# Kernel tuning notes

Hardware: AMD Instinct MI355X
Metric: run time of the kernel (lower is better)

## Reference

```python
import jax, jax.numpy as jnp
import numpy as np

# config
HIDDEN = 1024
NUM_EXPERTS = 16
TOP_K = 4
MOE_INTER = 512
NUM_SHARED = 2
SHARED_INTER = MOE_INTER * NUM_SHARED  # 1024
NORM_TOPK = True
ROUTED_SCALE = 1.0
NUM_TOKENS = 1024


def setup_inputs() -> dict:
    key = jax.random.key(0)
    ks = jax.random.split(key, 8)
    s = 0.02
    return {
        "hidden_states": jax.random.normal(ks[0], (NUM_TOKENS, HIDDEN), jnp.float32),
        # router (BailingMoEGate): weight [E, H], no bias
        "router_w": jax.random.normal(ks[1], (NUM_EXPERTS, HIDDEN), jnp.float32) * s,
        # routed experts: gate/up proj [E, H, I], down proj [E, I, H]
        "w_gate": jax.random.normal(ks[2], (NUM_EXPERTS, HIDDEN, MOE_INTER), jnp.float32) * s,
        "w_up": jax.random.normal(ks[3], (NUM_EXPERTS, HIDDEN, MOE_INTER), jnp.float32) * s,
        "w_down": jax.random.normal(ks[4], (NUM_EXPERTS, MOE_INTER, HIDDEN), jnp.float32) * s,
        # shared experts (BailingMoEMLP, merged gate_up): [H, 2*Is], [Is, H]
        "ws_gate_up": jax.random.normal(ks[5], (HIDDEN, 2 * SHARED_INTER), jnp.float32) * s,
        "ws_down": jax.random.normal(ks[6], (SHARED_INTER, HIDDEN), jnp.float32) * s,
    }


def _moe_forward(x, router_w, w_gate, w_up, w_down, ws_gate_up, ws_down):
    T = x.shape[0]
    # ---- router: logits -> softmax -> top-k (score_function='softmax', no bias)
    logits = jnp.einsum("th,eh->te", x, router_w)          # [T, E]
    probs = jax.nn.softmax(logits, axis=-1)
    topk_w, topk_idx = jax.lax.top_k(probs, TOP_K)         # [T, K]
    if NORM_TOPK:
        topk_w = topk_w / jnp.sum(topk_w, axis=-1, keepdims=True)
    topk_w = topk_w * ROUTED_SCALE
    # sparse combine weights [T, E] (zeros for non-selected experts)
    combine = jnp.zeros((T, NUM_EXPERTS), x.dtype).at[
        jnp.arange(T)[:, None], topk_idx
    ].set(topk_w.astype(x.dtype))
    # ---- routed experts: SiLU(x W_gate) * (x W_up) then W_down, weighted combine
    g = jnp.einsum("th,ehi->tei", x, w_gate)               # [T, E, I]
    u = jnp.einsum("th,ehi->tei", x, w_up)
    h = jax.nn.silu(g) * u
    routed = jnp.einsum("tei,eih,te->th", h, w_down, combine)
    # ---- shared experts (dense SwiGLU MLP)
    gu = x @ ws_gate_up                                    # [T, 2*Is]
    g_s, u_s = jnp.split(gu, 2, axis=-1)
    shared = (jax.nn.silu(g_s) * u_s) @ ws_down
    return routed + shared


def reference(hidden_states, router_w, w_gate, w_up, w_down, ws_gate_up, ws_down):
    return _moe_forward(hidden_states, router_w, w_gate, w_up, w_down,
                        ws_gate_up, ws_down)
```

## Files before the change

### kernel.cpp

```cpp
#include <hip/hip_runtime.h>
#include <stdint.h>


typedef __attribute__((ext_vector_type(8))) unsigned short ushort8;
typedef __attribute__((ext_vector_type(4))) float f32x4;
typedef __attribute__((ext_vector_type(8))) __bf16 bf16x8;

#define T_TOK 1024
#define HID   1024
#define NEXP  16
#define TOPK  4
#define MINTER 512
#define SINTER 1024

constexpr size_t OFF_COUNTS = 0;
constexpr size_t OFF_LIST   = 1024;
constexpr size_t OFF_WT     = OFF_LIST  + 65536;
constexpr size_t OFF_TIDX   = OFF_WT    + 65536;
constexpr size_t OFF_XB     = OFF_TIDX  + 65536;
constexpr size_t OFF_HS     = OFF_XB    + 2097152;
constexpr size_t OFF_HR     = OFF_HS    + 2097152;
constexpr size_t OFF_WGT    = OFF_HR    + 4194304;
constexpr size_t OFF_WUT    = OFF_WGT   + 16777216;
constexpr size_t OFF_WDT    = OFF_WUT   + 16777216;
constexpr size_t OFF_WSGUT  = OFF_WDT   + 16777216;
constexpr size_t OFF_WSDT   = OFF_WSGUT + 4194304;
constexpr size_t OFF_ROUT   = OFF_WGT;

__device__ __forceinline__ unsigned short f2bf(float f) {
  union { float f; uint32_t u; } v; v.f = f;
  uint32_t r = (v.u + 0x7FFFu + ((v.u >> 16) & 1u)) >> 16;
  return (unsigned short)r;
}
__device__ __forceinline__ bf16x8 as_bf16x8(ushort8 s) {
  union { ushort8 s; bf16x8 b; } u; u.s = s; return u.b;
}
__device__ __forceinline__ float silu(float g) { return g / (1.f + __expf(-g)); }

__device__ __forceinline__ void glds16(const unsigned short* g, unsigned short* l) {
  __builtin_amdgcn_global_load_lds(
      (const __attribute__((address_space(1))) unsigned int*)g,
      (__attribute__((address_space(3))) unsigned int*)l, 16, 0, 0);
}

__global__ void init_kernel(int* counts) {
  if (threadIdx.x < NEXP) counts[threadIdx.x] = 0;
}

__global__ __launch_bounds__(64) void router_kernel(
    const float* __restrict__ x, const float* __restrict__ rw,
    int* counts, int* list, float* wt, int* tIdx) {
  const int t = blockIdx.x, l = threadIdx.x;
  float xv[16];
#pragma unroll
  for (int j = 0; j < 16; j++) xv[j] = x[t * HID + j * 64 + l];
  float p[NEXP];
#pragma unroll
  for (int e = 0; e < NEXP; e++) {
    float s = 0.f;
#pragma unroll
    for (int j = 0; j < 16; j++) s += xv[j] * rw[e * HID + j * 64 + l];
#pragma unroll
    for (int off = 32; off > 0; off >>= 1) s += __shfl_xor(s, off);
    p[e] = s;
  }
  float mx = p[0];
#pragma unroll
  for (int e = 1; e < NEXP; e++) mx = fmaxf(mx, p[e]);
  int idx[TOPK]; float w4[TOPK]; float wsum = 0.f; unsigned used = 0u;
#pragma unroll
  for (int k = 0; k < TOPK; k++) {
    float bv = -1e30f; int bi = 0;
#pragma unroll
    for (int e = 0; e < NEXP; e++)
      if (!((used >> e) & 1u) && p[e] > bv) { bv = p[e]; bi = e; }
    used |= 1u << bi;
    idx[k] = bi;
    w4[k] = __expf(p[bi] - mx);
    wsum += w4[k];
  }
  const float inv = 1.f / wsum;
  if (l < TOPK) {
    const int e = idx[l];
    const int pos = atomicAdd(&counts[e], 1);
    list[e * 1024 + pos] = t;
    wt[e * 1024 + pos]   = w4[l] * inv;
    tIdx[t * TOPK + l]   = (e << 10) | pos;
  }
}

__global__ void convert_bf16_kernel(const float* __restrict__ src,
                                    unsigned short* __restrict__ dst, int n) {
  const int i = (blockIdx.x * blockDim.x + threadIdx.x) * 4;
  if (i + 3 < n) {
    const float4 v = *(const float4*)(src + i);
    dst[i + 0] = f2bf(v.x); dst[i + 1] = f2bf(v.y);
    dst[i + 2] = f2bf(v.z); dst[i + 3] = f2bf(v.w);
  }
}

__global__ __launch_bounds__(256) void transpose64_kernel(
    const float* __restrict__ src, unsigned short* __restrict__ dst,
    int R, int C) {
  __shared__ float tile[64][65];
  const size_t bo = (size_t)blockIdx.z * R * C;
  const int c0 = blockIdx.x * 64, r0 = blockIdx.y * 64, t = threadIdx.x;
  {
    const int r = t >> 4, c4 = (t & 15) * 4;
#pragma unroll
    for (int p = 0; p < 4; p++) {
      const int rr = p * 16 + r;
      const float4 v = *(const float4*)(src + bo + (size_t)(r0 + rr) * C + c0 + c4);
      tile[rr][c4 + 0] = v.x; tile[rr][c4 + 1] = v.y;
      tile[rr][c4 + 2] = v.z; tile[rr][c4 + 3] = v.w;
    }
  }
  __syncthreads();
  {
    const int c = t >> 2, rb = (t & 3) * 16;
#pragma unroll
    for (int s = 0; s < 4; s++) {
      const int rr = rb + 4 * s;
      union { unsigned short u[4]; uint2 v; } pk;
#pragma unroll
      for (int i = 0; i < 4; i++) pk.u[i] = f2bf(tile[rr + i][c]);
      *(uint2*)(dst + bo + (size_t)(c0 + c) * R + r0 + rr) = pk.v;
    }
  }
}

__global__ __launch_bounds__(256, 2) void phase1_kernel(
    const unsigned short* __restrict__ Xb,
    const unsigned short* __restrict__ WgT,
    const unsigned short* __restrict__ WuT,
    const unsigned short* __restrict__ WsguT,
    const int* __restrict__ counts, const int* __restrict__ list,
    const float* __restrict__ wt,
    unsigned short* __restrict__ Hr,
    unsigned short* __restrict__ Hs) {
  const int z = blockIdx.z, x = blockIdx.x, y = blockIdx.y;
  const bool routed = (z < NEXP);
  int cnt = 0, base = 0;
  if (routed) {
    if (x >= 4) return;
    cnt = counts[z];
    if (y * 128 >= cnt) return;
#pragma unroll
    for (int i = 0; i < NEXP; i++) base += (i < z) ? counts[i] : 0;
  }
  __shared__ __align__(16) unsigned short sA[128 * 64];
  __shared__ __align__(16) unsigned short sB[256 * 64];
  const int tid = threadIdx.x, w = tid >> 6, l = tid & 63;
  const int wm = w >> 1, wn = w & 1, m0 = y * 128;

  const int ar = tid >> 1;
  const unsigned short* aRow;
  if (routed) {
    const int pos = min(m0 + ar, cnt - 1);
    aRow = Xb + (size_t)list[z * 1024 + pos] * HID;
  } else {
    aRow = Xb + (size_t)(m0 + ar) * HID;
  }
  const unsigned short* aptr[4];
  int aoff[4];
#pragma unroll
  for (int c = 0; c < 4; c++) {
    const int p = (tid & 1) * 4 + c;
    aptr[c] = aRow + ((p ^ (ar & 7)) * 8);
    aoff[c] = ar * 64 + p * 8;
  }
  const unsigned short* bptr[8];
#pragma unroll
  for (int i = 0; i < 8; i++) {
    const int R = 64 * w + 8 * i + (l >> 3);
    const int g = (l & 7) ^ (R & 7);
    const unsigned short* rowp;
    if (routed) {
      const int col = x * 128 + (R & 127);
      rowp = ((R >> 7) ? WuT : WgT) + (size_t)z * MINTER * HID + (size_t)col * HID;
    } else {
      const int col = x * 128 + (R & 127);
      rowp = WsguT + (size_t)((R >> 7) * SINTER + col) * HID;
    }
    bptr[i] = rowp + g * 8;
  }

  f32x4 accG[4][4], accU[4][4];
#pragma unroll
  for (int i = 0; i < 4; i++)
#pragma unroll
    for (int j = 0; j < 4; j++) {
      accG[i][j] = (f32x4){0.f, 0.f, 0.f, 0.f};
      accU[i][j] = (f32x4){0.f, 0.f, 0.f, 0.f};
    }

  for (int k0 = 0; k0 < HID; k0 += 64) {
    ushort8 av[4];
#pragma unroll
    for (int c = 0; c < 4; c++) av[c] = *(const ushort8*)(aptr[c] + k0);
    __syncthreads();
#pragma unroll
    for (int c = 0; c < 4; c++) *(ushort8*)(sA + aoff[c]) = av[c];
#pragma unroll
    for (int i = 0; i < 8; i++)
      glds16(bptr[i] + k0, sB + (64 * w + 8 * i) * 64);
    __syncthreads();
#pragma unroll
    for (int h = 0; h < 2; h++) {
      const int pc = ((h * 4 + (l >> 4)) ^ (l & 7)) * 8;
      bf16x8 af[4];
#pragma unroll
      for (int i = 0; i < 4; i++)
        af[i] = as_bf16x8(*(const ushort8*)(sA + (wm * 64 + 16 * i + (l & 15)) * 64 + pc));
#pragma unroll
      for (int j = 0; j < 4; j++) {
        const int Rg = wn * 64 + 16 * j + (l & 15);
        const bf16x8 gf = as_bf16x8(*(const ushort8*)(sB + Rg * 64 + pc));
        const bf16x8 uf = as_bf16x8(*(const ushort8*)(sB + (128 + Rg) * 64 + pc));
#pragma unroll
        for (int i = 0; i < 4; i++) {
          accG[i][j] = __builtin_amdgcn_mfma_f32_16x16x32_bf16(af[i], gf, accG[i][j], 0, 0, 0);
          accU[i][j] = __builtin_amdgcn_mfma_f32_16x16x32_bf16(af[i], uf, accU[i][j], 0, 0, 0);
        }
      }
    }
  }

#pragma unroll
  for (int i = 0; i < 4; i++)
#pragma unroll
    for (int r = 0; r < 4; r++) {
      const int row = wm * 64 + 16 * i + (l >> 4) * 4 + r;
      const int grow = m0 + row;
      if (routed) {
        if (grow < cnt) {
          const float wrow = wt[z * 1024 + grow];
#pragma unroll
          for (int j = 0; j < 4; j++) {
            const int col = x * 128 + wn * 64 + 16 * j + (l & 15);
            const float h = silu(accG[i][j][r]) * accU[i][j][r] * wrow;
            Hr[(size_t)(base + grow) * MINTER + col] = f2bf(h);
          }
        }
      } else {
#pragma unroll
        for (int j = 0; j < 4; j++) {
          const int col = x * 128 + wn * 64 + 16 * j + (l & 15);
          const float h = silu(accG[i][j][r]) * accU[i][j][r];
          Hs[(size_t)grow * SINTER + col] = f2bf(h);
        }
      }
    }
}

__global__ __launch_bounds__(256, 2) void phase2_kernel(
    const unsigned short* __restrict__ Hr, const unsigned short* __restrict__ Hs,
    const unsigned short* __restrict__ WdT,
    const unsigned short* __restrict__ WsdT,
    const int* __restrict__ counts,
    float* __restrict__ Rout,
    float* __restrict__ out) {
  const int z = blockIdx.z, x = blockIdx.x, y = blockIdx.y;
  const bool routed = (z < NEXP);
  int cnt = 0, base = 0, kdim;
  if (routed) {
    cnt = counts[z];
    if (y * 128 >= cnt) return;
#pragma unroll
    for (int i = 0; i < NEXP; i++) base += (i < z) ? counts[i] : 0;
    kdim = MINTER;
  } else {
    kdim = SINTER;
  }
  __shared__ __align__(16) unsigned short sA[128 * 64];
  __shared__ __align__(16) unsigned short sB[256 * 64];
  const int tid = threadIdx.x, w = tid >> 6, l = tid & 63;
  const int wm = w >> 1, wn = w & 1, m0 = y * 128;

  const int ar = tid >> 1;
  const unsigned short* aRow;
  if (routed) {
    const int pos = min(m0 + ar, cnt - 1);
    aRow = Hr + (size_t)(base + pos) * MINTER;
  } else {
    aRow = Hs + (size_t)(m0 + ar) * SINTER;
  }
  const unsigned short* aptr[4];
  int aoff[4];
#pragma unroll
  for (int c = 0; c < 4; c++) {
    const int p = (tid & 1) * 4 + c;
    aptr[c] = aRow + ((p ^ (ar & 7)) * 8);
    aoff[c] = ar * 64 + p * 8;
  }
  const unsigned short* bptr[8];
#pragma unroll
  for (int i = 0; i < 8; i++) {
    const int R = 64 * w + 8 * i + (l >> 3);
    const int g = (l & 7) ^ (R & 7);
    const int col = x * 256 + R;
    const unsigned short* rowp =
        routed ? (WdT + (size_t)z * HID * MINTER + (size_t)col * MINTER)
               : (WsdT + (size_t)col * SINTER);
    bptr[i] = rowp + g * 8;
  }

  f32x4 acc[4][8];
#pragma unroll
  for (int i = 0; i < 4; i++)
#pragma unroll
    for (int j = 0; j < 8; j++) acc[i][j] = (f32x4){0.f, 0.f, 0.f, 0.f};

  for (int k0 = 0; k0 < kdim; k0 += 64) {
    ushort8 av[4];
#pragma unroll
    for (int c = 0; c < 4; c++) av[c] = *(const ushort8*)(aptr[c] + k0);
    __syncthreads();
#pragma unroll
    for (int c = 0; c < 4; c++) *(ushort8*)(sA + aoff[c]) = av[c];
#pragma unroll
    for (int i = 0; i < 8; i++)
      glds16(bptr[i] + k0, sB + (64 * w + 8 * i) * 64);
    __syncthreads();
#pragma unroll
    for (int h = 0; h < 2; h++) {
      const int pc = ((h * 4 + (l >> 4)) ^ (l & 7)) * 8;
      bf16x8 af[4];
#pragma unroll
      for (int i = 0; i < 4; i++)
        af[i] = as_bf16x8(*(const ushort8*)(sA + (wm * 64 + 16 * i + (l & 15)) * 64 + pc));
#pragma unroll
      for (int j = 0; j < 8; j++) {
        const int Rb = wn * 128 + 16 * j + (l & 15);
        const bf16x8 bfv = as_bf16x8(*(const ushort8*)(sB + Rb * 64 + pc));
#pragma unroll
        for (int i = 0; i < 4; i++)
          acc[i][j] = __builtin_amdgcn_mfma_f32_16x16x32_bf16(af[i], bfv, acc[i][j], 0, 0, 0);
      }
    }
  }

#pragma unroll
  for (int i = 0; i < 4; i++)
#pragma unroll
    for (int r = 0; r < 4; r++) {
      const int row = wm * 64 + 16 * i + (l >> 4) * 4 + r;
      const int grow = m0 + row;
      if (routed) {
        if (grow < cnt) {
#pragma unroll
          for (int j = 0; j < 8; j++) {
            const int col = x * 256 + wn * 128 + 16 * j + (l & 15);
            Rout[(size_t)(base + grow) * HID + col] = acc[i][j][r];
          }
        }
      } else {
#pragma unroll
        for (int j = 0; j < 8; j++) {
          const int col = x * 256 + wn * 128 + 16 * j + (l & 15);
          out[(size_t)grow * HID + col] = acc[i][j][r];
        }
      }
    }
}

__global__ __launch_bounds__(256) void combine_kernel(
    const float* __restrict__ Rout, const int* __restrict__ counts,
    const int* __restrict__ tIdx, float* __restrict__ out) {
  __shared__ int sb[NEXP];
  if (threadIdx.x == 0) {
    int s = 0;
#pragma unroll
    for (int e = 0; e < NEXP; e++) { sb[e] = s; s += counts[e]; }
  }
  __syncthreads();
  const int t = blockIdx.x, c4 = threadIdx.x * 4;
  float4 o = *(const float4*)(out + (size_t)t * HID + c4);
#pragma unroll
  for (int k = 0; k < TOPK; k++) {
    const int v = tIdx[t * TOPK + k];
    const int row = sb[v >> 10] + (v & 1023);
    const float4 rv = *(const float4*)(Rout + (size_t)row * HID + c4);
    o.x += rv.x; o.y += rv.y; o.z += rv.z; o.w += rv.w;
  }
  *(float4*)(out + (size_t)t * HID + c4) = o;
}

extern "C" void kernel_launch(void* const* d_in, const int* in_sizes, int n_in,
                              void* d_out, int out_size, void* d_ws, size_t ws_size,
                              hipStream_t stream) {
  const float* x      = (const float*)d_in[0];
  const float* rw     = (const float*)d_in[1];
  const float* w_gate = (const float*)d_in[2];
  const float* w_up   = (const float*)d_in[3];
  const float* w_down = (const float*)d_in[4];
  const float* ws_gu  = (const float*)d_in[5];
  const float* ws_dn  = (const float*)d_in[6];
  float* out = (float*)d_out;
  char* ws = (char*)d_ws;

  int*   counts = (int*)  (ws + OFF_COUNTS);
  int*   list   = (int*)  (ws + OFF_LIST);
  float* wtbuf  = (float*)(ws + OFF_WT);
  int*   tIdx   = (int*)  (ws + OFF_TIDX);
  unsigned short* Xb    = (unsigned short*)(ws + OFF_XB);
  unsigned short* Hs    = (unsigned short*)(ws + OFF_HS);
  unsigned short* Hr    = (unsigned short*)(ws + OFF_HR);
  unsigned short* WgT   = (unsigned short*)(ws + OFF_WGT);
  unsigned short* WuT   = (unsigned short*)(ws + OFF_WUT);
  unsigned short* WdT   = (unsigned short*)(ws + OFF_WDT);
  unsigned short* WsguT = (unsigned short*)(ws + OFF_WSGUT);
  unsigned short* WsdT  = (unsigned short*)(ws + OFF_WSDT);
  float* Rout = (float*)(ws + OFF_ROUT);

  init_kernel<<<1, 64, 0, stream>>>(counts);
  router_kernel<<<T_TOK, 64, 0, stream>>>(x, rw, counts, list, wtbuf, tIdx);
  convert_bf16_kernel<<<1024, 256, 0, stream>>>(x, Xb, T_TOK * HID);
  transpose64_kernel<<<dim3(8, 16, 16), 256, 0, stream>>>(w_gate, WgT, HID, MINTER);
  transpose64_kernel<<<dim3(8, 16, 16), 256, 0, stream>>>(w_up,   WuT, HID, MINTER);
  transpose64_kernel<<<dim3(16, 8, 16), 256, 0, stream>>>(w_down, WdT, MINTER, HID);
  transpose64_kernel<<<dim3(32, 16, 1), 256, 0, stream>>>(ws_gu,  WsguT, HID, 2 * SINTER);
  transpose64_kernel<<<dim3(16, 16, 1), 256, 0, stream>>>(ws_dn,  WsdT, SINTER, HID);
  phase1_kernel<<<dim3(8, 8, 17), 256, 0, stream>>>(
      Xb, WgT, WuT, WsguT, counts, list, wtbuf, Hr, Hs);
  phase2_kernel<<<dim3(4, 8, 17), 256, 0, stream>>>(
      Hr, Hs, WdT, WsdT, counts, Rout, out);
  combine_kernel<<<T_TOK, 256, 0, stream>>>(Rout, counts, tIdx, out);
  (void)in_sizes; (void)n_in; (void)out_size; (void)ws_size;
}
```

Before: 301.5 us.

## Double-buffer GEMM K-loop with async LDS loads, fuse prep kernels, bf16 routed output

```diff
diff --git a/kernel.cpp b/kernel.cpp
--- a/kernel.cpp
+++ b/kernel.cpp
@@ -32,6 +32,9 @@
   uint32_t r = (v.u + 0x7FFFu + ((v.u >> 16) & 1u)) >> 16;
   return (unsigned short)r;
 }
+__device__ __forceinline__ float bfu2f(uint32_t u) {
+  union { uint32_t u; float f; } v; v.u = u << 16; return v.f;
+}
 __device__ __forceinline__ bf16x8 as_bf16x8(ushort8 s) {
   union { ushort8 s; bf16x8 b; } u; u.s = s; return u.b;
 }
@@ -49,11 +52,14 @@
 
 __global__ __launch_bounds__(64) void router_kernel(
     const float* __restrict__ x, const float* __restrict__ rw,
-    int* counts, int* list, float* wt, int* tIdx) {
+    int* counts, int* list, float* wt, int* tIdx,
+    unsigned short* __restrict__ Xb) {
   const int t = blockIdx.x, l = threadIdx.x;
   float xv[16];
 #pragma unroll
   for (int j = 0; j < 16; j++) xv[j] = x[t * HID + j * 64 + l];
+#pragma unroll
+  for (int j = 0; j < 16; j++) Xb[t * HID + j * 64 + l] = f2bf(xv[j]);
   float p[NEXP];
 #pragma unroll
   for (int e = 0; e < NEXP; e++) {
@@ -89,22 +95,36 @@
   }
 }
 
-__global__ void convert_bf16_kernel(const float* __restrict__ src,
-                                    unsigned short* __restrict__ dst, int n) {
-  const int i = (blockIdx.x * blockDim.x + threadIdx.x) * 4;
-  if (i + 3 < n) {
-    const float4 v = *(const float4*)(src + i);
-    dst[i + 0] = f2bf(v.x); dst[i + 1] = f2bf(v.y);
-    dst[i + 2] = f2bf(v.z); dst[i + 3] = f2bf(v.w);
-  }
-}
-
-__global__ __launch_bounds__(256) void transpose64_kernel(
-    const float* __restrict__ src, unsigned short* __restrict__ dst,
-    int R, int C) {
+__global__ __launch_bounds__(256) void transpose_all_kernel(
+    const float* __restrict__ Wg, const float* __restrict__ Wu,
+    const float* __restrict__ Wd, const float* __restrict__ Wsgu,
+    const float* __restrict__ Wsd,
+    unsigned short* __restrict__ WgT, unsigned short* __restrict__ WuT,
+    unsigned short* __restrict__ WdT, unsigned short* __restrict__ WsguT,
+    unsigned short* __restrict__ WsdT) {
+  const int bid = blockIdx.x;
+  const float* src; unsigned short* dst; int R, C, tx, ty; size_t bo;
+  if (bid < 4096) {
+    const int which = bid >> 11, loc = bid & 2047;
+    const int b = loc >> 7, t8 = loc & 127;
+    src = which ? Wu : Wg; dst = which ? WuT : WgT;
+    R = 1024; C = 512; bo = (size_t)b * R * C;
+    tx = t8 & 7; ty = t8 >> 3;
+  } else if (bid < 6144) {
+    const int loc = bid - 4096, b = loc >> 7, t8 = loc & 127;
+    src = Wd; dst = WdT; R = 512; C = 1024; bo = (size_t)b * R * C;
+    tx = t8 & 15; ty = t8 >> 4;
+  } else if (bid < 6656) {
+    const int loc = bid - 6144;
+    src = Wsgu; dst = WsguT; R = 1024; C = 2048; bo = 0;
+    tx = loc & 31; ty = loc >> 5;
+  } else {
+    const int loc = bid - 6656;
+    src = Wsd; dst = WsdT; R = 1024; C = 1024; bo = 0;
+    tx = loc & 15; ty = loc >> 4;
+  }
   __shared__ float tile[64][65];
-  const size_t bo = (size_t)blockIdx.z * R * C;
-  const int c0 = blockIdx.x * 64, r0 = blockIdx.y * 64, t = threadIdx.x;
+  const int c0 = tx * 64, r0 = ty * 64, t = threadIdx.x;
   {
     const int r = t >> 4, c4 = (t & 15) * 4;
 #pragma unroll
@@ -148,41 +168,44 @@
 #pragma unroll
     for (int i = 0; i < NEXP; i++) base += (i < z) ? counts[i] : 0;
   }
-  __shared__ __align__(16) unsigned short sA[128 * 64];
-  __shared__ __align__(16) unsigned short sB[256 * 64];
+  __shared__ __align__(16) unsigned short sA[2][128 * 32];
+  __shared__ __align__(16) unsigned short sB[2][256 * 32];
   const int tid = threadIdx.x, w = tid >> 6, l = tid & 63;
   const int wm = w >> 1, wn = w & 1, m0 = y * 128;
-
-  const int ar = tid >> 1;
-  const unsigned short* aRow;
-  if (routed) {
-    const int pos = min(m0 + ar, cnt - 1);
-    aRow = Xb + (size_t)list[z * 1024 + pos] * HID;
-  } else {
-    aRow = Xb + (size_t)(m0 + ar) * HID;
-  }
-  const unsigned short* aptr[4];
-  int aoff[4];
-#pragma unroll
-  for (int c = 0; c < 4; c++) {
-    const int p = (tid & 1) * 4 + c;
-    aptr[c] = aRow + ((p ^ (ar & 7)) * 8);
-    aoff[c] = ar * 64 + p * 8;
-  }
-  const unsigned short* bptr[8];
-#pragma unroll
-  for (int i = 0; i < 8; i++) {
-    const int R = 64 * w + 8 * i + (l >> 3);
-    const int g = (l & 7) ^ (R & 7);
-    const unsigned short* rowp;
-    if (routed) {
-      const int col = x * 128 + (R & 127);
-      rowp = ((R >> 7) ? WuT : WgT) + (size_t)z * MINTER * HID + (size_t)col * HID;
-    } else {
-      const int col = x * 128 + (R & 127);
-      rowp = WsguT + (size_t)((R >> 7) * SINTER + col) * HID;
-    }
-    bptr[i] = rowp + g * 8;
+  const int lg = ((l & 3) ^ ((l >> 3) & 3)) * 8;
+
+  const unsigned short* aP[2];
+#pragma unroll
+  for (int ii = 0; ii < 2; ii++) {
+    const int r = (2 * w + ii) * 16 + (l >> 2);
+    const unsigned short* row;
+    if (routed) row = Xb + (size_t)list[z * 1024 + min(m0 + r, cnt - 1)] * HID;
+    else        row = Xb + (size_t)(m0 + r) * HID;
+    aP[ii] = row + lg;
+  }
+  const unsigned short* bP[4];
+#pragma unroll
+  for (int ii = 0; ii < 4; ii++) {
+    const int R = (4 * w + ii) * 16 + (l >> 2);
+    const int col = x * 128 + (R & 127);
+    const unsigned short* row;
+    if (routed)
+      row = ((R >= 128) ? WuT : WgT) + ((size_t)z * MINTER + col) * HID;
+    else
+      row = WsguT + ((size_t)((R >= 128) ? SINTER : 0) + col) * HID;
+    bP[ii] = row + lg;
+  }
+
+  int aoff[4], boff[4];
+#pragma unroll
+  for (int i = 0; i < 4; i++) {
+    const int m = wm * 64 + 16 * i + (l & 15);
+    aoff[i] = m * 32 + (((l >> 4) ^ ((m >> 1) & 3)) * 8);
+  }
+#pragma unroll
+  for (int j = 0; j < 4; j++) {
+    const int n = wn * 64 + 16 * j + (l & 15);
+    boff[j] = n * 32 + (((l >> 4) ^ ((n >> 1) & 3)) * 8);
   }
 
   f32x4 accG[4][4], accU[4][4];
@@ -194,34 +217,32 @@
       accU[i][j] = (f32x4){0.f, 0.f, 0.f, 0.f};
     }
 
-  for (int k0 = 0; k0 < HID; k0 += 64) {
-    ushort8 av[4];
-#pragma unroll
-    for (int c = 0; c < 4; c++) av[c] = *(const ushort8*)(aptr[c] + k0);
+  auto stage = [&](int k0, int bi) {
+    unsigned short* A = sA[bi]; unsigned short* B = sB[bi];
+#pragma unroll
+    for (int ii = 0; ii < 2; ii++) glds16(aP[ii] + k0, A + (2 * w + ii) * 512);
+#pragma unroll
+    for (int ii = 0; ii < 4; ii++) glds16(bP[ii] + k0, B + (4 * w + ii) * 512);
+  };
+
+  stage(0, 0);
+  const int steps = HID / 32;
+  for (int s = 0; s < steps; s++) {
     __syncthreads();
-#pragma unroll
-    for (int c = 0; c < 4; c++) *(ushort8*)(sA + aoff[c]) = av[c];
-#pragma unroll
-    for (int i = 0; i < 8; i++)
-      glds16(bptr[i] + k0, sB + (64 * w + 8 * i) * 64);
-    __syncthreads();
-#pragma unroll
-    for (int h = 0; h < 2; h++) {
-      const int pc = ((h * 4 + (l >> 4)) ^ (l & 7)) * 8;
-      bf16x8 af[4];
-#pragma unroll
-      for (int i = 0; i < 4; i++)
-        af[i] = as_bf16x8(*(const ushort8*)(sA + (wm * 64 + 16 * i + (l & 15)) * 64 + pc));
-#pragma unroll
-      for (int j = 0; j < 4; j++) {
-        const int Rg = wn * 64 + 16 * j + (l & 15);
-        const bf16x8 gf = as_bf16x8(*(const ushort8*)(sB + Rg * 64 + pc));
-        const bf16x8 uf = as_bf16x8(*(const ushort8*)(sB + (128 + Rg) * 64 + pc));
-#pragma unroll
-        for (int i = 0; i < 4; i++) {
-          accG[i][j] = __builtin_amdgcn_mfma_f32_16x16x32_bf16(af[i], gf, accG[i][j], 0, 0, 0);
-          accU[i][j] = __builtin_amdgcn_mfma_f32_16x16x32_bf16(af[i], uf, accU[i][j], 0, 0, 0);
-        }
+    if (s + 1 < steps) stage((s + 1) * 32, (s + 1) & 1);
+    const unsigned short* A = sA[s & 1];
+    const unsigned short* B = sB[s & 1];
+    bf16x8 af[4];
+#pragma unroll
+    for (int i = 0; i < 4; i++) af[i] = as_bf16x8(*(const ushort8*)(A + aoff[i]));
+#pragma unroll
+    for (int j = 0; j < 4; j++) {
+      const bf16x8 gf = as_bf16x8(*(const ushort8*)(B + boff[j]));
+      const bf16x8 uf = as_bf16x8(*(const ushort8*)(B + 128 * 32 + boff[j]));
+#pragma unroll
+      for (int i = 0; i < 4; i++) {
+        accG[i][j] = __builtin_amdgcn_mfma_f32_16x16x32_bf16(af[i], gf, accG[i][j], 0, 0, 0);
+        accU[i][j] = __builtin_amdgcn_mfma_f32_16x16x32_bf16(af[i], uf, accU[i][j], 0, 0, 0);
       }
     }
   }
@@ -258,7 +279,7 @@
     const unsigned short* __restrict__ WdT,
     const unsigned short* __restrict__ WsdT,
     const int* __restrict__ counts,
-    float* __restrict__ Rout,
+    unsigned short* __restrict__ Rout,
     float* __restrict__ out) {
   const int z = blockIdx.z, x = blockIdx.x, y = blockIdx.y;
   const bool routed = (z < NEXP);
@@ -272,37 +293,42 @@
   } else {
     kdim = SINTER;
   }
-  __shared__ __align__(16) unsigned short sA[128 * 64];
-  __shared__ __align__(16) unsigned short sB[256 * 64];
+  __shared__ __align__(16) unsigned short sA[2][128 * 32];
+  __shared__ __align__(16) unsigned short sB[2][256 * 32];
   const int tid = threadIdx.x, w = tid >> 6, l = tid & 63;
   const int wm = w >> 1, wn = w & 1, m0 = y * 128;
-
-  const int ar = tid >> 1;
-  const unsigned short* aRow;
-  if (routed) {
-    const int pos = min(m0 + ar, cnt - 1);
-    aRow = Hr + (size_t)(base + pos) * MINTER;
-  } else {
-    aRow = Hs + (size_t)(m0 + ar) * SINTER;
-  }
-  const unsigned short* aptr[4];
-  int aoff[4];
-#pragma unroll
-  for (int c = 0; c < 4; c++) {
-    const int p = (tid & 1) * 4 + c;
-    aptr[c] = aRow + ((p ^ (ar & 7)) * 8);
-    aoff[c] = ar * 64 + p * 8;
-  }
-  const unsigned short* bptr[8];
-#pragma unroll
-  for (int i = 0; i < 8; i++) {
-    const int R = 64 * w + 8 * i + (l >> 3);
-    const int g = (l & 7) ^ (R & 7);
+  const int lg = ((l & 3) ^ ((l >> 3) & 3)) * 8;
+
+  const unsigned short* aP[2];
+#pragma unroll
+  for (int ii = 0; ii < 2; ii++) {
+    const int r = (2 * w + ii) * 16 + (l >> 2);
+    const unsigned short* row;
+    if (routed) row = Hr + (size_t)(base + min(m0 + r, cnt - 1)) * MINTER;
+    else        row = Hs + (size_t)(m0 + r) * SINTER;
+    aP[ii] = row + lg;
+  }
+  const unsigned short* bP[4];
+#pragma unroll
+  for (int ii = 0; ii < 4; ii++) {
+    const int R = (4 * w + ii) * 16 + (l >> 2);
     const int col = x * 256 + R;
-    const unsigned short* rowp =
-        routed ? (WdT + (size_t)z * HID * MINTER + (size_t)col * MINTER)
+    const unsigned short* row =
+        routed ? (WdT + ((size_t)z * HID + col) * MINTER)
                : (WsdT + (size_t)col * SINTER);
-    bptr[i] = rowp + g * 8;
+    bP[ii] = row + lg;
+  }
+
+  int aoff[4], boff[8];
+#pragma unroll
+  for (int i = 0; i < 4; i++) {
+    const int m = wm * 64 + 16 * i + (l & 15);
+    aoff[i] = m * 32 + (((l >> 4) ^ ((m >> 1) & 3)) * 8);
+  }
+#pragma unroll
+  for (int j = 0; j < 8; j++) {
+    const int n = wn * 128 + 16 * j + (l & 15);
+    boff[j] = n * 32 + (((l >> 4) ^ ((n >> 1) & 3)) * 8);
   }
 
   f32x4 acc[4][8];
@@ -311,32 +337,30 @@
 #pragma unroll
     for (int j = 0; j < 8; j++) acc[i][j] = (f32x4){0.f, 0.f, 0.f, 0.f};
 
-  for (int k0 = 0; k0 < kdim; k0 += 64) {
-    ushort8 av[4];
-#pragma unroll
-    for (int c = 0; c < 4; c++) av[c] = *(const ushort8*)(aptr[c] + k0);
+  auto stage = [&](int k0, int bi) {
+    unsigned short* A = sA[bi]; unsigned short* B = sB[bi];
+#pragma unroll
+    for (int ii = 0; ii < 2; ii++) glds16(aP[ii] + k0, A + (2 * w + ii) * 512);
+#pragma unroll
+    for (int ii = 0; ii < 4; ii++) glds16(bP[ii] + k0, B + (4 * w + ii) * 512);
+  };
+
+  stage(0, 0);
+  const int steps = kdim / 32;
+  for (int s = 0; s < steps; s++) {
     __syncthreads();
-#pragma unroll
-    for (int c = 0; c < 4; c++) *(ushort8*)(sA + aoff[c]) = av[c];
-#pragma unroll
-    for (int i = 0; i < 8; i++)
-      glds16(bptr[i] + k0, sB + (64 * w + 8 * i) * 64);
-    __syncthreads();
-#pragma unroll
-    for (int h = 0; h < 2; h++) {
-      const int pc = ((h * 4 + (l >> 4)) ^ (l & 7)) * 8;
-      bf16x8 af[4];
+    if (s + 1 < steps) stage((s + 1) * 32, (s + 1) & 1);
+    const unsigned short* A = sA[s & 1];
+    const unsigned short* B = sB[s & 1];
+    bf16x8 af[4];
+#pragma unroll
+    for (int i = 0; i < 4; i++) af[i] = as_bf16x8(*(const ushort8*)(A + aoff[i]));
+#pragma unroll
+    for (int j = 0; j < 8; j++) {
+      const bf16x8 bfv = as_bf16x8(*(const ushort8*)(B + boff[j]));
 #pragma unroll
       for (int i = 0; i < 4; i++)
-        af[i] = as_bf16x8(*(const ushort8*)(sA + (wm * 64 + 16 * i + (l & 15)) * 64 + pc));
-#pragma unroll
-      for (int j = 0; j < 8; j++) {
-        const int Rb = wn * 128 + 16 * j + (l & 15);
-        const bf16x8 bfv = as_bf16x8(*(const ushort8*)(sB + Rb * 64 + pc));
-#pragma unroll
-        for (int i = 0; i < 4; i++)
-          acc[i][j] = __builtin_amdgcn_mfma_f32_16x16x32_bf16(af[i], bfv, acc[i][j], 0, 0, 0);
-      }
+        acc[i][j] = __builtin_amdgcn_mfma_f32_16x16x32_bf16(af[i], bfv, acc[i][j], 0, 0, 0);
     }
   }
 
@@ -351,7 +375,7 @@
 #pragma unroll
           for (int j = 0; j < 8; j++) {
             const int col = x * 256 + wn * 128 + 16 * j + (l & 15);
-            Rout[(size_t)(base + grow) * HID + col] = acc[i][j][r];
+            Rout[(size_t)(base + grow) * HID + col] = f2bf(acc[i][j][r]);
           }
         }
       } else {
@@ -365,7 +389,7 @@
 }
 
 __global__ __launch_bounds__(256) void combine_kernel(
-    const float* __restrict__ Rout, const int* __restrict__ counts,
+    const unsigned short* __restrict__ Rout, const int* __restrict__ counts,
     const int* __restrict__ tIdx, float* __restrict__ out) {
   __shared__ int sb[NEXP];
   if (threadIdx.x == 0) {
@@ -380,8 +404,9 @@
   for (int k = 0; k < TOPK; k++) {
     const int v = tIdx[t * TOPK + k];
     const int row = sb[v >> 10] + (v & 1023);
-    const float4 rv = *(const float4*)(Rout + (size_t)row * HID + c4);
-    o.x += rv.x; o.y += rv.y; o.z += rv.z; o.w += rv.w;
+    const uint2 rv = *(const uint2*)(Rout + (size_t)row * HID + c4);
+    o.x += bfu2f(rv.x & 0xffffu); o.y += bfu2f(rv.x >> 16);
+    o.z += bfu2f(rv.y & 0xffffu); o.w += bfu2f(rv.y >> 16);
   }
   *(float4*)(out + (size_t)t * HID + c4) = o;
 }
@@ -411,16 +436,12 @@
   unsigned short* WdT   = (unsigned short*)(ws + OFF_WDT);
   unsigned short* WsguT = (unsigned short*)(ws + OFF_WSGUT);
   unsigned short* WsdT  = (unsigned short*)(ws + OFF_WSDT);
-  float* Rout = (float*)(ws + OFF_ROUT);
+  unsigned short* Rout  = (unsigned short*)(ws + OFF_ROUT);
 
   init_kernel<<<1, 64, 0, stream>>>(counts);
-  router_kernel<<<T_TOK, 64, 0, stream>>>(x, rw, counts, list, wtbuf, tIdx);
-  convert_bf16_kernel<<<1024, 256, 0, stream>>>(x, Xb, T_TOK * HID);
-  transpose64_kernel<<<dim3(8, 16, 16), 256, 0, stream>>>(w_gate, WgT, HID, MINTER);
-  transpose64_kernel<<<dim3(8, 16, 16), 256, 0, stream>>>(w_up,   WuT, HID, MINTER);
-  transpose64_kernel<<<dim3(16, 8, 16), 256, 0, stream>>>(w_down, WdT, MINTER, HID);
-  transpose64_kernel<<<dim3(32, 16, 1), 256, 0, stream>>>(ws_gu,  WsguT, HID, 2 * SINTER);
-  transpose64_kernel<<<dim3(16, 16, 1), 256, 0, stream>>>(ws_dn,  WsdT, SINTER, HID);
+  router_kernel<<<T_TOK, 64, 0, stream>>>(x, rw, counts, list, wtbuf, tIdx, Xb);
+  transpose_all_kernel<<<6912, 256, 0, stream>>>(
+      w_gate, w_up, w_down, ws_gu, ws_dn, WgT, WuT, WdT, WsguT, WsdT);
   phase1_kernel<<<dim3(8, 8, 17), 256, 0, stream>>>(
       Xb, WgT, WuT, WsguT, counts, list, wtbuf, Hr, Hs);
   phase2_kernel<<<dim3(4, 8, 17), 256, 0, stream>>>(
```

New measurement: 296.3 us. Within noise of the previous version (-1.7%).
